# Optimization experiments

Measured on AMD Instinct MI355X. Metric: run time of the kernel, lower is better.

Reference implementation:

```python
import jax, jax.numpy as jnp
import numpy as np

B, T, N, H = 512, 128, 128, 256


def setup_inputs() -> dict:
    key = jax.random.key(0)
    ks = jax.random.split(key, 8)
    rn = lambda k, shape, sc: (jax.random.normal(k, shape, jnp.float32) * sc)
    return {
        "data": rn(ks[0], (B, T, N), 1.0),
        "h0": jnp.zeros((B, H), jnp.float32),
        # SimpleRNNCell params: h_t = tanh(x@Wx + h@Wh + b)
        "Wx": rn(ks[1], (N, H), 0.05),
        "Wh": rn(ks[2], (H, H), 0.05),
        "b": jnp.zeros((H,), jnp.float32),
        # InputAttention: w1: Dense(T) over last dim T; w2: Dense(T) over hidden; v: Dense(1)
        "W1": rn(ks[3], (T, T), 0.05),
        "b1": jnp.zeros((T,), jnp.float32),
        "W2": rn(ks[4], (H, T), 0.05),
        "b2": jnp.zeros((T,), jnp.float32),
        "Wv": rn(ks[5], (T, 1), 0.05),
        "bv": jnp.zeros((1,), jnp.float32),
        "n": N,
    }


def reference(data, h0, Wx, Wh, b, W1, b1, W2, b2, Wv, bv, n):
    # data: (B, T, n); h0: (B, H)
    Tlen = data.shape[1]
    x_perm = jnp.swapaxes(data, 1, 2)          # (B, n, T) == Permute((2,1))(x)
    pre = x_perm @ W1 + b1                      # w1(x_perm): loop-invariant, hoisted

    def step(h, x_t):
        # SimpleRNNCell: new state used for this step's attention
        h_new = jnp.tanh(x_t @ Wx + h @ Wh + b)                 # (B, H)
        q = h_new @ W2 + b2                                      # w2(RepeatVector(n)(h)) per row -> (B, T)
        score = jnp.tanh(pre + q[:, None, :])                    # (B, n, T)
        e = score @ Wv + bv                                      # (B, n, 1)
        e = jnp.swapaxes(e, 1, 2)                                # Permute((2,1)) -> (B, 1, n)
        alpha = jax.nn.softmax(e, axis=-1)                       # softmax over n
        return h_new, alpha

    xs = jnp.swapaxes(data, 0, 1)               # (T, B, n): data[:, t, :] per step
    _, alphas = jax.lax.scan(step, h0, xs)      # (T, B, 1, n)
    # faithful to tf.reshape(alpha_seq.stack(), (-1, T, n))
    alpha_seq = alphas.reshape(-1, Tlen, n)     # (B, T, n)
    return data * alpha_seq
```

## Files before the change

### kernel.cpp

```cpp
#include <hip/hip_runtime.h>


#define C2L 2.8853900817779268f
#define L2E 1.4426950408889634f

typedef _Float16 hf;
typedef _Float16 hf2 __attribute__((ext_vector_type(2)));
typedef _Float16 hf4 __attribute__((ext_vector_type(4)));
typedef _Float16 hf8 __attribute__((ext_vector_type(8)));
typedef float f32x4 __attribute__((ext_vector_type(4)));

__device__ __forceinline__ float fast_exp2(float x){
#if __has_builtin(__builtin_amdgcn_exp2f)
  return __builtin_amdgcn_exp2f(x);
#else
  return exp2f(x);
#endif
}
__device__ __forceinline__ float fast_rcp(float x){
#if __has_builtin(__builtin_amdgcn_rcpf)
  return __builtin_amdgcn_rcpf(x);
#else
  return 1.f/x;
#endif
}
__device__ __forceinline__ float dot2f(hf2 a, hf2 b, float c){
#if __has_builtin(__builtin_amdgcn_fdot2)
  return __builtin_amdgcn_fdot2(a, b, c, false);
#else
  return c + (float)a.x*(float)b.x + (float)a.y*(float)b.y;
#endif
}

__global__ __launch_bounds__(256) void k_prep_w(const float* __restrict__ Wx,
    const float* __restrict__ W2, const float* __restrict__ W1,
    hf* __restrict__ wts){
  int tid = blockIdx.x*256 + threadIdx.x;
  if (tid < 32768){
    int n = tid >> 7, k = tid & 127;
    wts[tid] = (hf)Wx[k*256 + n];
  } else if (tid < 65536){
    int t2 = tid - 32768;
    int n = t2 >> 8, k = t2 & 255;
    wts[tid] = (hf)W2[k*128 + n];
  } else {
    int t3 = tid - 65536;
    int n = t3 >> 7, k = t3 & 127;
    wts[tid] = (hf)W1[k*128 + n];
  }
}

template<int K, int MODE>
__global__ __launch_bounds__(256) void k_gemm(const void* __restrict__ Asrc,
    const hf* __restrict__ Bt, const float* __restrict__ bias,
    float* __restrict__ Cout){
  constexpr int SA = 136;
  __shared__ alignas(16) hf As[64*SA];
  __shared__ alignas(16) hf Bs[128*SA];
  const int tid = threadIdx.x;
  const int w = tid >> 6, lane = tid & 63;
  const int c = lane & 15, q = lane >> 4;
  const int bx = blockIdx.x;
  const int col0 = (MODE==0) ? blockIdx.y*128 : 0;

  float br[8];
  #pragma unroll
  for (int ni=0; ni<8; ni++) br[ni] = bias[col0 + ni*16 + c];

  f32x4 acc[8];
  #pragma unroll
  for (int ni=0; ni<8; ni++) acc[ni] = (f32x4){0.f,0.f,0.f,0.f};

  for (int kc=0; kc<K/128; kc++){
    if (MODE == 0){
      const float* A = (const float*)Asrc + (long)bx*64*128;
      #pragma unroll
      for (int v=0; v<8; v++){
        int f4 = v*256 + tid;
        int m = f4 >> 5, k4 = (f4 & 31)*4;
        float4 d = *(const float4*)&A[m*128 + k4];
        hf4 h = {(hf)d.x,(hf)d.y,(hf)d.z,(hf)d.w};
        *(hf4*)&As[m*SA + k4] = h;
      }
    } else if (MODE == 1){
      const hf* A = (const hf*)Asrc + (long)bx*64*256;
      #pragma unroll
      for (int v=0; v<4; v++){
        int f8 = v*256 + tid;
        int m = f8 >> 4, k8 = (f8 & 15)*8;
        *(hf8*)&As[m*SA + k8] = *(const hf8*)&A[m*256 + kc*128 + k8];
      }
    } else {
      const float* A = (const float*)Asrc + (long)(bx>>1)*16384;
      const int i0 = (bx & 1)*64;
      #pragma unroll
      for (int v=0; v<8; v++){
        int f4 = v*256 + tid;
        int t = f4 >> 4, i4 = (f4 & 15)*4;
        float4 d = *(const float4*)&A[t*128 + i0 + i4];
        As[(i4+0)*SA + t] = (hf)d.x;
        As[(i4+1)*SA + t] = (hf)d.y;
        As[(i4+2)*SA + t] = (hf)d.z;
        As[(i4+3)*SA + t] = (hf)d.w;
      }
    }
    #pragma unroll
    for (int v=0; v<8; v++){
      int f8 = v*256 + tid;
      int n = f8 >> 4, k8 = (f8 & 15)*8;
      *(hf8*)&Bs[n*SA + k8] = *(const hf8*)&Bt[(col0+n)*K + kc*128 + k8];
    }
    __syncthreads();
    #pragma unroll
    for (int kk=0; kk<4; kk++){
      hf8 a = *(const hf8*)&As[(w*16 + c)*SA + kk*32 + q*8];
      #pragma unroll
      for (int ni=0; ni<8; ni++){
        hf8 b = *(const hf8*)&Bs[(ni*16 + c)*SA + kk*32 + q*8];
        acc[ni] = __builtin_amdgcn_mfma_f32_16x16x32_f16(a, b, acc[ni], 0, 0, 0);
      }
    }
    __syncthreads();
  }
  #pragma unroll
  for (int ni=0; ni<8; ni++){
    #pragma unroll
    for (int r=0; r<4; r++){
      int rloc = w*16 + q*4 + r;
      int col = col0 + ni*16 + c;
      float val = acc[ni][r] + br[ni];
      int addr;
      if (MODE == 0){
        int R = bx*64 + rloc;
        int b_ = R >> 7, t_ = R & 127;
        addr = (t_*512 + b_)*256 + col;
      } else if (MODE == 1){
        int R = bx*64 + rloc;
        addr = R*128 + col;
        val = fast_exp2(C2L*val);
      } else {
        int b_ = bx >> 1, i_ = (bx & 1)*64 + rloc;
        addr = b_*16384 + i_*128 + col;
        val = fast_exp2(C2L*val);
      }
      Cout[addr] = val;
    }
  }
}

__global__ __launch_bounds__(256, 3) void k_rnn(const float* __restrict__ h0,
    const float* __restrict__ Wh, const float* __restrict__ xw,
    hf* __restrict__ Hb){
  __shared__ alignas(16) hf h_s[2][256];
  const int j = threadIdx.x;
  const int bb = blockIdx.x;
  hf2 wreg[128];
  #pragma unroll
  for (int m=0;m<128;m++){
    float w0 = Wh[(2*m)*256 + j];
    float w1 = Wh[(2*m+1)*256 + j];
    wreg[m] = (hf2){(hf)w0, (hf)w1};
  }
  h_s[0][j] = (hf)h0[bb*256 + j];
  float z = xw[(0*512 + bb)*256 + j];
  __syncthreads();
  for (int t=0;t<128;t++){
    int p = t & 1;
    float zn = (t < 127) ? xw[((t+1)*512 + bb)*256 + j] : 0.f;
    const hf8* h8 = (const hf8*)(&h_s[p][0]);
    float a[8];
    #pragma unroll
    for (int u=0;u<8;u++) a[u]=0.f;
    #pragma unroll
    for (int mm=0; mm<32; mm++){
      hf8 hv = h8[mm];
      hf2 h0p = {hv[0],hv[1]}, h1p = {hv[2],hv[3]};
      hf2 h2p = {hv[4],hv[5]}, h3p = {hv[6],hv[7]};
      a[(4*mm+0)&7] = dot2f(wreg[4*mm+0], h0p, a[(4*mm+0)&7]);
      a[(4*mm+1)&7] = dot2f(wreg[4*mm+1], h1p, a[(4*mm+1)&7]);
      a[(4*mm+2)&7] = dot2f(wreg[4*mm+2], h2p, a[(4*mm+2)&7]);
      a[(4*mm+3)&7] = dot2f(wreg[4*mm+3], h3p, a[(4*mm+3)&7]);
    }
    float v = z + (((a[0]+a[1])+(a[2]+a[3])) + ((a[4]+a[5])+(a[6]+a[7])));
    float e2 = fast_exp2(v*C2L);
    float hn = 1.f - 2.f*fast_rcp(e2 + 1.f);
    Hb[(t*512+bb)*256 + j] = (hf)hn;
    h_s[p^1][j] = (hf)hn;
    z = zn;
    __syncthreads();
  }
}

__global__ __launch_bounds__(256, 4) void k_attn(const float* __restrict__ P,
    const float* __restrict__ Qm, const float* __restrict__ Wv,
    const float* __restrict__ data, float* __restrict__ out){
  __shared__ alignas(16) float qs[32*128];
  __shared__ alignas(16) float wvs[128];
  __shared__ alignas(16) float epart[2][2][4][128];
  __shared__ float red[2][4][2];
  const int b = blockIdx.x, tile = blockIdx.y;
  const int tid = threadIdx.x;
  const int i = tid & 127, hl = tid >> 7;
  const int t0 = tile*32;
  if (tid < 128) wvs[tid] = -2.f*Wv[tid];
  #pragma unroll
  for (int v=0; v<4; v++){
    int flat = v*1024 + tid*4;
    int tt = flat >> 7, c = flat & 127;
    *(float4*)&qs[flat] = *(const float4*)&Qm[((t0+tt)*512 + b)*128 + c];
  }
  float4 p4[16];
  const float* prow = P + b*16384 + i*128 + hl*64;
  #pragma unroll
  for (int v=0; v<16; v++) p4[v] = *(const float4*)&prow[v*4];
  __syncthreads();
  for (int tp=0; tp<8; tp++){
    const int pp = tp & 1;
    const float* q0r = &qs[(4*tp)*128   + hl*64];
    const float* q1r = &qs[(4*tp+1)*128 + hl*64];
    const float* q2r = &qs[(4*tp+2)*128 + hl*64];
    const float* q3r = &qs[(4*tp+3)*128 + hl*64];
    const float* wvr = &wvs[hl*64];
    float acc0=0.f, acc1=0.f, acc2=0.f, acc3=0.f;
    #pragma unroll
    for (int m=0; m<16; m++){
      float4 Pv = p4[m];
      float4 wv = *(const float4*)&wvr[m*4];
      {
        float4 qq = *(const float4*)&q0r[m*4];
        float u = fmaf(Pv.x, qq.x, 1.f), v = fmaf(Pv.y, qq.y, 1.f);
        float n = fmaf(wv.x, v, wv.y*u);
        acc0 = fmaf(n, fast_rcp(u*v), acc0);
        float u2 = fmaf(Pv.z, qq.z, 1.f), v2 = fmaf(Pv.w, qq.w, 1.f);
        float n2 = fmaf(wv.z, v2, wv.w*u2);
        acc0 = fmaf(n2, fast_rcp(u2*v2), acc0);
      }
      {
        float4 qq = *(const float4*)&q1r[m*4];
        float u = fmaf(Pv.x, qq.x, 1.f), v = fmaf(Pv.y, qq.y, 1.f);
        float n = fmaf(wv.x, v, wv.y*u);
        acc1 = fmaf(n, fast_rcp(u*v), acc1);
        float u2 = fmaf(Pv.z, qq.z, 1.f), v2 = fmaf(Pv.w, qq.w, 1.f);
        float n2 = fmaf(wv.z, v2, wv.w*u2);
        acc1 = fmaf(n2, fast_rcp(u2*v2), acc1);
      }
      {
        float4 qq = *(const float4*)&q2r[m*4];
        float u = fmaf(Pv.x, qq.x, 1.f), v = fmaf(Pv.y, qq.y, 1.f);
        float n = fmaf(wv.x, v, wv.y*u);
        acc2 = fmaf(n, fast_rcp(u*v), acc2);
        float u2 = fmaf(Pv.z, qq.z, 1.f), v2 = fmaf(Pv.w, qq.w, 1.f);
        float n2 = fmaf(wv.z, v2, wv.w*u2);
        acc2 = fmaf(n2, fast_rcp(u2*v2), acc2);
      }
      {
        float4 qq = *(const float4*)&q3r[m*4];
        float u = fmaf(Pv.x, qq.x, 1.f), v = fmaf(Pv.y, qq.y, 1.f);
        float n = fmaf(wv.x, v, wv.y*u);
        acc3 = fmaf(n, fast_rcp(u*v), acc3);
        float u2 = fmaf(Pv.z, qq.z, 1.f), v2 = fmaf(Pv.w, qq.w, 1.f);
        float n2 = fmaf(wv.z, v2, wv.w*u2);
        acc3 = fmaf(n2, fast_rcp(u2*v2), acc3);
      }
    }
    epart[pp][hl][0][i] = acc0;
    epart[pp][hl][1][i] = acc1;
    epart[pp][hl][2][i] = acc2;
    epart[pp][hl][3][i] = acc3;
    __syncthreads();
    const int g = tid >> 7;
    float pe[2];
    #pragma unroll
    for (int s=0; s<2; s++){
      int tl = g + 2*s;
      float e = epart[pp][0][tl][i] + epart[pp][1][tl][i];
      pe[s] = fast_exp2(e*L2E);
      float sm = pe[s];
      #pragma unroll
      for (int off=32; off; off>>=1) sm += __shfl_xor(sm, off);
      if ((tid & 63) == 0) red[pp][tl][(tid>>6)&1] = sm;
    }
    __syncthreads();
    #pragma unroll
    for (int s=0; s<2; s++){
      int tl = g + 2*s;
      float ssum = red[pp][tl][0] + red[pp][tl][1];
      float alpha = pe[s] * fast_rcp(ssum);
      int t = t0 + 4*tp + tl;
      int base = (t*512 + b)*128 + i;
      out[base] = data[base]*alpha;
    }
  }
}

extern "C" void kernel_launch(void* const* d_in, const int* in_sizes, int n_in,
                              void* d_out, int out_size, void* d_ws, size_t ws_size,
                              hipStream_t stream) {
  const float* data = (const float*)d_in[0];
  const float* h0   = (const float*)d_in[1];
  const float* Wx   = (const float*)d_in[2];
  const float* Wh   = (const float*)d_in[3];
  const float* bb   = (const float*)d_in[4];
  const float* W1   = (const float*)d_in[5];
  const float* b1   = (const float*)d_in[6];
  const float* W2   = (const float*)d_in[7];
  const float* b2   = (const float*)d_in[8];
  const float* Wv   = (const float*)d_in[9];
  float* wsp = (float*)d_ws;
  float* P   = wsp;
  float* xwQ = wsp + 8388608;
  hf*    Hbf = (hf*)(wsp + 25165824);
  hf*    wts = (hf*)(wsp + 33554432);
  const hf* Wxt = wts;
  const hf* W2t = wts + 32768;
  const hf* W1t = wts + 65536;
  float* out = (float*)d_out;

  hipLaunchKernelGGL(k_prep_w, dim3(320), dim3(256), 0, stream, Wx, W2, W1, wts);
  hipLaunchKernelGGL((k_gemm<128,0>), dim3(1024,2), dim3(256), 0, stream,
                     (const void*)data, Wxt, bb, xwQ);
  hipLaunchKernelGGL((k_gemm<128,2>), dim3(1024),   dim3(256), 0, stream,
                     (const void*)data, W1t, b1, P);
  hipLaunchKernelGGL(k_rnn, dim3(512), dim3(256), 0, stream, h0, Wh, xwQ, Hbf);
  hipLaunchKernelGGL((k_gemm<256,1>), dim3(1024),   dim3(256), 0, stream,
                     (const void*)Hbf, W2t, b2, xwQ);
  hipLaunchKernelGGL(k_attn, dim3(512, 4), dim3(256), 0, stream, P, xwQ, Wv, data, out);
}
```

Before: 385.5 us.

## Batch the RNN recurrence on MFMA and fuse the W2 projection into it

The per-row scalar dot2 RNN kernel is replaced by one where each 512-thread block handles 16 batch rows. It computes h@Wh with 16x16x32 f16 MFMAs from pre-transposed half-precision Wh held in registers. The W2 query projection and its exp transform now run inside the recurrence, one step behind, so the separate GEMM and the fp16 hidden-state buffer round trip go away. The barrier waits only on LDS counters. The grid shrinks to 32 blocks, which leaves most CUs idle during the serial recurrence.

```diff
diff --git a/kernel.cpp b/kernel.cpp
--- a/kernel.cpp
+++ b/kernel.cpp
@@ -24,17 +24,14 @@
   return 1.f/x;
 #endif
 }
-__device__ __forceinline__ float dot2f(hf2 a, hf2 b, float c){
-#if __has_builtin(__builtin_amdgcn_fdot2)
-  return __builtin_amdgcn_fdot2(a, b, c, false);
-#else
-  return c + (float)a.x*(float)b.x + (float)a.y*(float)b.y;
-#endif
+__device__ __forceinline__ void sync_lds_only(){
+  asm volatile("s_waitcnt lgkmcnt(0)" ::: "memory");
+  __builtin_amdgcn_s_barrier();
 }
 
 __global__ __launch_bounds__(256) void k_prep_w(const float* __restrict__ Wx,
     const float* __restrict__ W2, const float* __restrict__ W1,
-    hf* __restrict__ wts){
+    const float* __restrict__ Wh, hf* __restrict__ wts){
   int tid = blockIdx.x*256 + threadIdx.x;
   if (tid < 32768){
     int n = tid >> 7, k = tid & 127;
@@ -43,11 +40,22 @@
     int t2 = tid - 32768;
     int n = t2 >> 8, k = t2 & 255;
     wts[tid] = (hf)W2[k*128 + n];
-  } else {
+  } else if (tid < 81920){
     int t3 = tid - 65536;
     int n = t3 >> 7, k = t3 & 127;
-    wts[tid] = (hf)W1[k*128 + n];
-  }
+    wts[tid] = (hf)W1[k*256 - k*128 + n];
+  } else {
+    int t4 = tid - 81920;
+    int n = t4 >> 8, k = t4 & 255;
+    wts[tid] = (hf)Wh[k*256 + n];
+  }
+}
+
+__global__ __launch_bounds__(256) void k_prep_w1(const float* __restrict__ W1,
+    hf* __restrict__ W1t){
+  int tid = blockIdx.x*256 + threadIdx.x;
+  int n = tid >> 7, k = tid & 127;
+  W1t[tid] = (hf)W1[k*128 + n];
 }
 
 template<int K, int MODE>
@@ -82,14 +90,6 @@
         hf4 h = {(hf)d.x,(hf)d.y,(hf)d.z,(hf)d.w};
         *(hf4*)&As[m*SA + k4] = h;
       }
-    } else if (MODE == 1){
-      const hf* A = (const hf*)Asrc + (long)bx*64*256;
-      #pragma unroll
-      for (int v=0; v<4; v++){
-        int f8 = v*256 + tid;
-        int m = f8 >> 4, k8 = (f8 & 15)*8;
-        *(hf8*)&As[m*SA + k8] = *(const hf8*)&A[m*256 + kc*128 + k8];
-      }
     } else {
       const float* A = (const float*)Asrc + (long)(bx>>1)*16384;
       const int i0 = (bx & 1)*64;
@@ -134,10 +134,6 @@
         int R = bx*64 + rloc;
         int b_ = R >> 7, t_ = R & 127;
         addr = (t_*512 + b_)*256 + col;
-      } else if (MODE == 1){
-        int R = bx*64 + rloc;
-        addr = R*128 + col;
-        val = fast_exp2(C2L*val);
       } else {
         int b_ = bx >> 1, i_ = (bx & 1)*64 + rloc;
         addr = b_*16384 + i_*128 + col;
@@ -148,46 +144,92 @@
   }
 }
 
-__global__ __launch_bounds__(256, 3) void k_rnn(const float* __restrict__ h0,
-    const float* __restrict__ Wh, const float* __restrict__ xw,
-    hf* __restrict__ Hb){
-  __shared__ alignas(16) hf h_s[2][256];
-  const int j = threadIdx.x;
-  const int bb = blockIdx.x;
-  hf2 wreg[128];
-  #pragma unroll
-  for (int m=0;m<128;m++){
-    float w0 = Wh[(2*m)*256 + j];
-    float w1 = Wh[(2*m+1)*256 + j];
-    wreg[m] = (hf2){(hf)w0, (hf)w1};
-  }
-  h_s[0][j] = (hf)h0[bb*256 + j];
-  float z = xw[(0*512 + bb)*256 + j];
-  __syncthreads();
-  for (int t=0;t<128;t++){
-    int p = t & 1;
-    float zn = (t < 127) ? xw[((t+1)*512 + bb)*256 + j] : 0.f;
-    const hf8* h8 = (const hf8*)(&h_s[p][0]);
-    float a[8];
-    #pragma unroll
-    for (int u=0;u<8;u++) a[u]=0.f;
-    #pragma unroll
-    for (int mm=0; mm<32; mm++){
-      hf8 hv = h8[mm];
-      hf2 h0p = {hv[0],hv[1]}, h1p = {hv[2],hv[3]};
-      hf2 h2p = {hv[4],hv[5]}, h3p = {hv[6],hv[7]};
-      a[(4*mm+0)&7] = dot2f(wreg[4*mm+0], h0p, a[(4*mm+0)&7]);
-      a[(4*mm+1)&7] = dot2f(wreg[4*mm+1], h1p, a[(4*mm+1)&7]);
-      a[(4*mm+2)&7] = dot2f(wreg[4*mm+2], h2p, a[(4*mm+2)&7]);
-      a[(4*mm+3)&7] = dot2f(wreg[4*mm+3], h3p, a[(4*mm+3)&7]);
-    }
-    float v = z + (((a[0]+a[1])+(a[2]+a[3])) + ((a[4]+a[5])+(a[6]+a[7])));
-    float e2 = fast_exp2(v*C2L);
-    float hn = 1.f - 2.f*fast_rcp(e2 + 1.f);
-    Hb[(t*512+bb)*256 + j] = (hf)hn;
-    h_s[p^1][j] = (hf)hn;
-    z = zn;
-    __syncthreads();
+__global__ __launch_bounds__(512, 2) void k_rnn(const float* __restrict__ h0,
+    const hf* __restrict__ Wht, const hf* __restrict__ W2t,
+    const float* __restrict__ b2, const float* __restrict__ xw,
+    float* __restrict__ Q){
+  constexpr int SK = 264;
+  __shared__ alignas(16) hf hs[2][16*SK];
+  const int tid = threadIdx.x;
+  const int w = tid >> 6, lane = tid & 63;
+  const int c = lane & 15, q = lane >> 4;
+  const int bb0 = blockIdx.x*16;
+  const int jb = w*32 + c;
+  const int tau = w*16 + c;
+
+  hf8 bf[2][8];
+  #pragma unroll
+  for (int ntl=0; ntl<2; ntl++)
+    #pragma unroll
+    for (int kc=0; kc<8; kc++)
+      bf[ntl][kc] = *(const hf8*)&Wht[(jb + ntl*16)*256 + kc*32 + q*8];
+  hf8 wf[8];
+  #pragma unroll
+  for (int kc=0; kc<8; kc++)
+    wf[kc] = *(const hf8*)&W2t[tau*256 + kc*32 + q*8];
+  const float b2v = b2[tau];
+
+  {
+    int m = tid >> 5, k0 = (tid & 31)*8;
+    const float* src = h0 + (bb0 + m)*256 + k0;
+    float4 u = *(const float4*)&src[0];
+    float4 v = *(const float4*)&src[4];
+    hf8 hh = {(hf)u.x,(hf)u.y,(hf)u.z,(hf)u.w,(hf)v.x,(hf)v.y,(hf)v.z,(hf)v.w};
+    *(hf8*)&hs[0][m*SK + k0] = hh;
+  }
+
+  float xwp[2][8];
+  #pragma unroll
+  for (int ntl=0; ntl<2; ntl++)
+    #pragma unroll
+    for (int r=0; r<4; r++)
+      xwp[0][ntl*4+r] = xw[(bb0 + q*4 + r)*256 + jb + ntl*16];
+  sync_lds_only();
+
+  for (int t=0; t<=128; t++){
+    const int cur = t & 1;
+    if (t < 128){
+      int tp1 = (t < 127) ? t+1 : 0;
+      #pragma unroll
+      for (int ntl=0; ntl<2; ntl++)
+        #pragma unroll
+        for (int r=0; r<4; r++)
+          xwp[cur^1][ntl*4+r] = xw[((tp1*512) + bb0 + q*4 + r)*256 + jb + ntl*16];
+    }
+    f32x4 acc0 = {0.f,0.f,0.f,0.f}, acc1 = {0.f,0.f,0.f,0.f};
+    f32x4 qac  = {0.f,0.f,0.f,0.f};
+    const hf* hrow = &hs[cur][0] + c*SK + q*8;
+    #pragma unroll
+    for (int kc=0; kc<8; kc++){
+      hf8 af = *(const hf8*)(hrow + kc*32);
+      if (t > 0)
+        qac = __builtin_amdgcn_mfma_f32_16x16x32_f16(af, wf[kc], qac, 0,0,0);
+      if (t < 128){
+        acc0 = __builtin_amdgcn_mfma_f32_16x16x32_f16(af, bf[0][kc], acc0, 0,0,0);
+        acc1 = __builtin_amdgcn_mfma_f32_16x16x32_f16(af, bf[1][kc], acc1, 0,0,0);
+      }
+    }
+    if (t > 0){
+      #pragma unroll
+      for (int r=0; r<4; r++){
+        float qv = fast_exp2(C2L*(qac[r] + b2v));
+        Q[((t-1)*512 + bb0 + q*4 + r)*128 + tau] = qv;
+      }
+    }
+    if (t < 128){
+      #pragma unroll
+      for (int ntl=0; ntl<2; ntl++){
+        f32x4 a = ntl ? acc1 : acc0;
+        #pragma unroll
+        for (int r=0; r<4; r++){
+          float v = a[r] + xwp[cur][ntl*4+r];
+          float e2 = fast_exp2(v*C2L);
+          float hn = 1.f - 2.f*fast_rcp(e2 + 1.f);
+          hs[cur^1][(q*4+r)*SK + jb + ntl*16] = (hf)hn;
+        }
+      }
+    }
+    sync_lds_only();
   }
 }
 
@@ -307,22 +349,23 @@
   const float* b2   = (const float*)d_in[8];
   const float* Wv   = (const float*)d_in[9];
   float* wsp = (float*)d_ws;
-  float* P   = wsp;
-  float* xwQ = wsp + 8388608;
-  hf*    Hbf = (hf*)(wsp + 25165824);
-  hf*    wts = (hf*)(wsp + 33554432);
-  const hf* Wxt = wts;
-  const hf* W2t = wts + 32768;
-  const hf* W1t = wts + 65536;
+  float* P    = wsp;
+  float* xw   = wsp + 8388608;
+  float* Qbuf = wsp + 25165824;
+  hf*    wts  = (hf*)(wsp + 33554432);
+  hf*    Wxt  = wts;
+  hf*    W2t  = wts + 32768;
+  hf*    W1t  = wts + 65536;
+  hf*    Wht  = wts + 81920;
   float* out = (float*)d_out;
 
-  hipLaunchKernelGGL(k_prep_w, dim3(320), dim3(256), 0, stream, Wx, W2, W1, wts);
+  hipLaunchKernelGGL(k_prep_w, dim3(576), dim3(256), 0, stream, Wx, W2, W1, Wh, wts);
+  hipLaunchKernelGGL(k_prep_w1, dim3(64), dim3(256), 0, stream, W1, W1t);
   hipLaunchKernelGGL((k_gemm<128,0>), dim3(1024,2), dim3(256), 0, stream,
-                     (const void*)data, Wxt, bb, xwQ);
+                     (const void*)data, Wxt, bb, xw);
   hipLaunchKernelGGL((k_gemm<128,2>), dim3(1024),   dim3(256), 0, stream,
                      (const void*)data, W1t, b1, P);
-  hipLaunchKernelGGL(k_rnn, dim3(512), dim3(256), 0, stream, h0, Wh, xwQ, Hbf);
-  hipLaunchKernelGGL((k_gemm<256,1>), dim3(1024),   dim3(256), 0, stream,
-                     (const void*)Hbf, W2t, b2, xwQ);
-  hipLaunchKernelGGL(k_attn, dim3(512, 4), dim3(256), 0, stream, P, xwQ, Wv, data, out);
-}
+  hipLaunchKernelGGL(k_rnn, dim3(32), dim3(512), 0, stream,
+                     h0, Wht, W2t, b2, xw, Qbuf);
+  hipLaunchKernelGGL(k_attn, dim3(512, 4), dim3(256), 0, stream, P, Qbuf, Wv, data, out);
+}
```

After: 455.1 us. 1.18x slower.
